# Kernel tuning notes

Hardware: AMD Instinct MI355X
Metric: run time of the kernel (lower is better)

The kernel has to match this reference:

```python
import jax, jax.numpy as jnp
import numpy as np

D_MODEL = 1024
NUM_HEADS = 16
HEAD_DIM = D_MODEL // NUM_HEADS
NUM_KERNELS = 21


def tisa_bias(amp, off, sharp, seq_len):
    # amp/off/sharp: (H, K). Returns (H, L, L) translation-invariant bias.
    # Evaluate on the 2L-1 distinct relative distances, then gather (Toeplitz).
    d = jnp.arange(-(seq_len - 1), seq_len, dtype=amp.dtype)  # (2L-1,)
    # (H, K, 2L-1) -> sum over kernels -> (H, 2L-1)
    scores = jnp.sum(
        amp[:, :, None]
        * jnp.exp(-jnp.abs(sharp)[:, :, None] * (d[None, None, :] - off[:, :, None]) ** 2),
        axis=1,
    )
    i = jnp.arange(seq_len)
    rel_idx = i[None, :] - i[:, None] + (seq_len - 1)  # (L, L) in [0, 2L-2]
    return scores[:, rel_idx]  # (H, L, L)


def setup_inputs() -> dict:
    key = jax.random.key(0)
    ks = jax.random.split(key, 9)
    B, L = 4, 1024
    s = 0.02
    return {
        "x_q": jax.random.normal(ks[0], (B, L, D_MODEL), dtype=jnp.float32),
        "x_kv": jax.random.normal(ks[1], (B, L, D_MODEL), dtype=jnp.float32),
        "Wq": jax.random.normal(ks[2], (D_MODEL, D_MODEL), dtype=jnp.float32) * s,
        "Wm": jax.random.normal(ks[3], (D_MODEL, 2 * D_MODEL), dtype=jnp.float32) * s,
        "Wg": jax.random.normal(ks[4], (D_MODEL, 2 * D_MODEL), dtype=jnp.float32) * s,
        "bg": jnp.zeros((2 * D_MODEL,), dtype=jnp.float32),
        "tisa_amp": jax.random.normal(ks[5], (NUM_HEADS, NUM_KERNELS), dtype=jnp.float32) * 0.1,
        "tisa_off": jax.random.uniform(ks[6], (NUM_HEADS, NUM_KERNELS), dtype=jnp.float32, minval=-512.0, maxval=512.0),
        "tisa_sharp": jax.random.uniform(ks[7], (NUM_HEADS, NUM_KERNELS), dtype=jnp.float32, minval=1e-4, maxval=0.05),
    }


def reference(x_q, x_kv, Wq, Wm, Wg, bg, tisa_amp, tisa_off, tisa_sharp):
    B, Lq, _ = x_q.shape
    Lkv = x_kv.shape[1]
    H, Dh = NUM_HEADS, HEAD_DIM

    q = (x_q @ Wq).reshape(B, Lq, H, Dh).transpose(0, 2, 1, 3)        # (B,H,Lq,Dh)
    mem = (x_kv @ Wm)                                                 # (B,Lkv,2D)
    k = mem[..., :D_MODEL].reshape(B, Lkv, H, Dh).transpose(0, 2, 1, 3)
    v = mem[..., D_MODEL:].reshape(B, Lkv, H, Dh).transpose(0, 2, 1, 3)

    scale = 1.0 / jnp.sqrt(jnp.asarray(Dh, dtype=q.dtype))
    scores = jnp.einsum("bhqd,bhkd->bhqk", q, k) * scale              # (B,H,Lq,Lkv)
    scores = scores + tisa_bias(tisa_amp, tisa_off, tisa_sharp, Lkv)[None]
    weights = jax.nn.softmax(scores, axis=-1)

    attn = jnp.einsum("bhqk,bhkd->bhqd", weights, v)                  # (B,H,Lq,Dh)
    attn = attn.transpose(0, 2, 1, 3).reshape(B, Lq, D_MODEL)

    g = attn @ Wg + bg                                                # (B,Lq,2D)
    a, b = g[..., :D_MODEL], g[..., D_MODEL:]
    return a * jax.nn.sigmoid(b)
```

## Files before the change

kernel.cpp:

```cpp
#include <hip/hip_runtime.h>
#include <cstdint>
#include <cstddef>

typedef __attribute__((ext_vector_type(8))) short bf16x8;
typedef __attribute__((ext_vector_type(4))) float f32x4;

#define LOG2E 1.44269504f

__device__ __forceinline__ unsigned short f2bf(float x) {
  unsigned int u = __float_as_uint(x);
  u += 0x7FFFu + ((u >> 16) & 1u);
  return (unsigned short)(u >> 16);
}
__device__ __forceinline__ unsigned short f2bf_trunc(float x) {
  return (unsigned short)(__float_as_uint(x) >> 16);
}

__device__ __forceinline__ bf16x8 pack8(const float4& a, const float4& b) {
  bf16x8 r;
  r[0] = (short)f2bf(a.x); r[1] = (short)f2bf(a.y);
  r[2] = (short)f2bf(a.z); r[3] = (short)f2bf(a.w);
  r[4] = (short)f2bf(b.x); r[5] = (short)f2bf(b.y);
  r[6] = (short)f2bf(b.z); r[7] = (short)f2bf(b.w);
  return r;
}

__device__ __forceinline__ void gload_lds16(const void* g, void* l) {
  __builtin_amdgcn_global_load_lds(
      (const __attribute__((address_space(1))) unsigned int*)g,
      (__attribute__((address_space(3))) unsigned int*)l, 16, 0, 0);
}


__global__ void preproc(const float* __restrict__ Wq, const float* __restrict__ Wm,
                        const float* __restrict__ Wg,
                        const float* __restrict__ amp, const float* __restrict__ off,
                        const float* __restrict__ sharp,
                        unsigned short* __restrict__ dWq, unsigned short* __restrict__ dWm,
                        unsigned short* __restrict__ dWg, float* __restrict__ tab) {
  __shared__ float tile[32][33];
  const int blk = blockIdx.x;
  if (blk < 6144) {
    int idx = blk;
    int z = idx >> 11, rem = idx & 2047;
    int bx = rem & 63, by = rem >> 6;
    const float* src = z == 0 ? Wq : (z == 1 ? Wm : Wg);
    unsigned short* dst = z == 0 ? dWq : (z == 1 ? dWm : dWg);
    int N = z == 0 ? 1024 : 2048;
    int nb = bx * 32, kb = by * 32;
    if (nb >= N) return;
    int tx = threadIdx.x & 31, ty = threadIdx.x >> 5;
#pragma unroll
    for (int r = ty; r < 32; r += 8)
      tile[r][tx] = src[(size_t)(kb + r) * N + nb + tx];
    __syncthreads();
#pragma unroll
    for (int r = ty; r < 32; r += 8)
      dst[(size_t)(nb + r) * 1024 + kb + tx] = f2bf(tile[tx][r]);
  } else {
    int h = blk - 6144;
    for (int idx = threadIdx.x; idx < 2047; idx += 256) {
      float d = (float)(idx - 1023);
      float acc = 0.f;
#pragma unroll
      for (int k = 0; k < 21; ++k) {
        float dd = d - off[h * 21 + k];
        acc += amp[h * 21 + k] * __expf(-fabsf(sharp[h * 21 + k]) * dd * dd);
      }
      tab[h * 2047 + idx] = acc * LOG2E;
    }
  }
}


template <int MODE>
__global__ __launch_bounds__(256, 3)
void qkv128(const float* __restrict__ X, const unsigned short* __restrict__ WT,
            unsigned short* __restrict__ qbuf, unsigned short* __restrict__ kbuf,
            unsigned short* __restrict__ vtbuf) {
  __shared__ unsigned short sA[3][128 * 32];
  __shared__ unsigned short sB[3][128 * 32];
  const int ntile = blockIdx.y << 7;
  const int mtile = blockIdx.x << 7;
  const int t = threadIdx.x, lane = t & 63, w = t >> 6;
  const int wm = w >> 1, wn = w & 1;
  const int c = lane & 15, g = lane >> 4;

  const int sr = t >> 2;
  const int sch = (t & 3) ^ ((sr >> 1) & 3);
  const float* aP0 = X + (size_t)(mtile + sr) * 1024 + sch * 8;
  const float* aP1 = aP0 + 64 * 1024;
  const unsigned short* bP0 = WT + (size_t)(ntile + sr) * 1024 + sch * 8;
  const unsigned short* bP1 = bP0 + 64 * 1024;
  const int lw = t * 8;

  float4 pA[4], iA[4];
  bf16x8 pB[2], iB[2];
  {
    float4 c0 = *(const float4*)(aP0);
    float4 c1 = *(const float4*)(aP0 + 4);
    float4 c2 = *(const float4*)(aP1);
    float4 c3 = *(const float4*)(aP1 + 4);
    bf16x8 cB0 = *(const bf16x8*)(bP0);
    bf16x8 cB1 = *(const bf16x8*)(bP1);
    pA[0] = *(const float4*)(aP0 + 32);
    pA[1] = *(const float4*)(aP0 + 36);
    pA[2] = *(const float4*)(aP1 + 32);
    pA[3] = *(const float4*)(aP1 + 36);
    pB[0] = *(const bf16x8*)(bP0 + 32);
    pB[1] = *(const bf16x8*)(bP1 + 32);
    *(bf16x8*)&sA[0][lw]        = pack8(c0, c1);
    *(bf16x8*)&sA[0][2048 + lw] = pack8(c2, c3);
    *(bf16x8*)&sB[0][lw]        = cB0;
    *(bf16x8*)&sB[0][2048 + lw] = cB1;
  }
  asm volatile("s_waitcnt lgkmcnt(0)" ::: "memory");
  __builtin_amdgcn_sched_barrier(0);
  asm volatile("s_barrier" ::: "memory");

  const int gx = (g ^ ((c >> 1) & 3)) * 8;
  const int aoff = (wm * 64 + c) * 32 + gx;
  const int boff = (wn * 64 + c) * 32 + gx;

  f32x4 acc[4][4] = {};
  int s0 = 0, s1 = 1, s2 = 2;

  for (int kt = 0; kt < 32; ++kt) {
    if (kt + 2 < 32) {
      const int ko = (kt + 2) * 32;
      iA[0] = *(const float4*)(aP0 + ko);
      iA[1] = *(const float4*)(aP0 + ko + 4);
      iA[2] = *(const float4*)(aP1 + ko);
      iA[3] = *(const float4*)(aP1 + ko + 4);
      iB[0] = *(const bf16x8*)(bP0 + ko);
      iB[1] = *(const bf16x8*)(bP1 + ko);
    }

    const unsigned short* sAp = &sA[s0][0];
    const unsigned short* sBc = &sB[s0][0];
    bf16x8 af[4], bfr[4];
#pragma unroll
    for (int i = 0; i < 4; ++i) af[i]  = *(const bf16x8*)&sAp[aoff + i * 512];
#pragma unroll
    for (int j = 0; j < 4; ++j) bfr[j] = *(const bf16x8*)&sBc[boff + j * 512];

    __builtin_amdgcn_s_setprio(1);
#pragma unroll
    for (int i = 0; i < 4; ++i)
#pragma unroll
      for (int j = 0; j < 4; ++j)
        acc[i][j] = __builtin_amdgcn_mfma_f32_16x16x32_bf16(af[i], bfr[j], acc[i][j], 0, 0, 0);
    __builtin_amdgcn_s_setprio(0);

    if (kt + 1 < 32) {
      *(bf16x8*)&sA[s1][lw]        = pack8(pA[0], pA[1]);
      *(bf16x8*)&sA[s1][2048 + lw] = pack8(pA[2], pA[3]);
      *(bf16x8*)&sB[s1][lw]        = pB[0];
      *(bf16x8*)&sB[s1][2048 + lw] = pB[1];
    }
#pragma unroll
    for (int q = 0; q < 4; ++q) pA[q] = iA[q];
    pB[0] = iB[0]; pB[1] = iB[1];

    asm volatile("s_waitcnt lgkmcnt(0)" ::: "memory");
    __builtin_amdgcn_sched_barrier(0);
    asm volatile("s_barrier" ::: "memory");
    __builtin_amdgcn_sched_barrier(0);

    int tmp = s0; s0 = s1; s1 = s2; s2 = tmp;
  }

  const int row0 = mtile + wm * 64 + (g << 2);
  const int col0 = ntile + wn * 64 + c;
  if (MODE == 0) {
#pragma unroll
    for (int i = 0; i < 4; ++i)
#pragma unroll
      for (int j = 0; j < 4; ++j) {
        int r = row0 + i * 16, cl = col0 + j * 16;
#pragma unroll
        for (int ri = 0; ri < 4; ++ri)
          qbuf[(size_t)(r + ri) * 1024 + cl] = f2bf(acc[i][j][ri] * (0.125f * LOG2E));
      }
  } else if (ntile < 1024) {
#pragma unroll
    for (int i = 0; i < 4; ++i)
#pragma unroll
      for (int j = 0; j < 4; ++j) {
        int r = row0 + i * 16, cl = col0 + j * 16;
#pragma unroll
        for (int ri = 0; ri < 4; ++ri)
          kbuf[(size_t)(r + ri) * 1024 + cl] = f2bf(acc[i][j][ri]);
      }
  } else {
#pragma unroll
    for (int i = 0; i < 4; ++i)
#pragma unroll
      for (int j = 0; j < 4; ++j) {
        int r = row0 + i * 16, cl = col0 + j * 16;
        int d = cl - 1024;
        int hh = d >> 6, dh = d & 63;
        int bb2 = r >> 10, ll = r & 1023;
        ushort4 pk;
        pk.x = f2bf(acc[i][j][0]);
        pk.y = f2bf(acc[i][j][1]);
        pk.z = f2bf(acc[i][j][2]);
        pk.w = f2bf(acc[i][j][3]);
        *(ushort4*)&vtbuf[((size_t)((bb2 * 16 + hh) * 64 + dh) << 10) + ll] = pk;
      }
  }
}


__global__ __launch_bounds__(512)
void attn_kernel(const unsigned short* __restrict__ qbuf,
                 const unsigned short* __restrict__ kbuf,
                 const unsigned short* __restrict__ vtbuf,
                 const float* __restrict__ biasTab,
                 unsigned short* __restrict__ attnb) {
  const int h = blockIdx.x & 15, b = blockIdx.x >> 4, qt = blockIdx.y;
  __shared__ unsigned short sK[2][64 * 64];
  __shared__ unsigned short sV[3][64 * 64];
  __shared__ unsigned short sP[2][128 * 64];
  __shared__ float sLsum[2][128];
  const int t = threadIdx.x, lane = t & 63, w = t >> 6;
  const int c = lane & 15, g = lane >> 4;
  const int rg = w >> 1, cg = w & 1;

  const int r = t >> 3, ch = (t & 7) ^ (r & 7);

  const unsigned short* qsrc = qbuf + (size_t)(b * 1024 + qt * 128) * 1024 + h * 64;
  const unsigned short* ksrc = kbuf + (size_t)(b * 1024) * 1024 + h * 64;
  const unsigned short* vsrc = vtbuf + (size_t)((b * 16 + h) * 64) * 1024;

  unsigned short* sQ = &sP[0][0];
  gload_lds16(qsrc + (size_t)r * 1024 + ch * 8, &sQ[t * 8]);
  gload_lds16(qsrc + (size_t)(r + 64) * 1024 + ch * 8, &sQ[4096 + t * 8]);
  gload_lds16(ksrc + (size_t)r * 1024 + ch * 8, &sK[0][t * 8]);
  gload_lds16(vsrc + (size_t)r * 1024 + ch * 8, &sV[0][t * 8]);

  const float* bb = biasTab + h * 2047 + 1023 + cg * 32 + c - qt * 128 - rg * 32 - g * 4;

  float bc[2][2][4];
#pragma unroll
  for (int rf = 0; rf < 2; ++rf)
#pragma unroll
    for (int nf = 0; nf < 2; ++nf)
#pragma unroll
      for (int ri = 0; ri < 4; ++ri)
        bc[rf][nf][ri] = bb[(nf - rf) * 16 - ri];

  __syncthreads();

  bf16x8 aq[2][2];
#pragma unroll
  for (int rf = 0; rf < 2; ++rf) {
    int row = rg * 32 + rf * 16 + c;
#pragma unroll
    for (int ks = 0; ks < 2; ++ks)
      aq[rf][ks] = *(const bf16x8*)&sQ[row * 64 + (((ks * 4 + g) ^ (row & 7)) * 8)];
  }
  __syncthreads();

  f32x4 o[2][2] = {};
  float lsum[2][4] = {};

  int vcur = 0, vnx = 1;
  for (int kv = 0; kv < 16; ++kv) {
    const int cur = kv & 1;

    f32x4 s[2][2];
#pragma unroll
    for (int rf = 0; rf < 2; ++rf)
#pragma unroll
      for (int nf = 0; nf < 2; ++nf)
#pragma unroll
        for (int ri = 0; ri < 4; ++ri)
          s[rf][nf][ri] = bc[rf][nf][ri];

    if (kv + 1 < 16) {
      gload_lds16(ksrc + (size_t)((kv + 1) * 64 + r) * 1024 + ch * 8, &sK[1 - cur][t * 8]);
      gload_lds16(vsrc + (size_t)r * 1024 + (kv + 1) * 64 + ch * 8, &sV[vnx][t * 8]);
      const float* bk = bb + (kv + 1) * 64;
#pragma unroll
      for (int rf = 0; rf < 2; ++rf)
#pragma unroll
        for (int nf = 0; nf < 2; ++nf)
#pragma unroll
          for (int ri = 0; ri < 4; ++ri)
            bc[rf][nf][ri] = bk[(nf - rf) * 16 - ri];
    }

#pragma unroll
    for (int nf = 0; nf < 2; ++nf) {
      int krow = cg * 32 + nf * 16 + c;
      bf16x8 k0 = *(const bf16x8*)&sK[cur][krow * 64 + (((g) ^ (krow & 7)) * 8)];
      bf16x8 k1 = *(const bf16x8*)&sK[cur][krow * 64 + (((4 + g) ^ (krow & 7)) * 8)];
#pragma unroll
      for (int rf = 0; rf < 2; ++rf) {
        s[rf][nf] = __builtin_amdgcn_mfma_f32_16x16x32_bf16(aq[rf][0], k0, s[rf][nf], 0, 0, 0);
        s[rf][nf] = __builtin_amdgcn_mfma_f32_16x16x32_bf16(aq[rf][1], k1, s[rf][nf], 0, 0, 0);
      }
    }

#pragma unroll
    for (int rf = 0; rf < 2; ++rf)
#pragma unroll
      for (int nf = 0; nf < 2; ++nf)
#pragma unroll
        for (int ri = 0; ri < 4; ++ri) {
          float e = exp2f(s[rf][nf][ri]);
          lsum[rf][ri] += e;
          int prow = rg * 32 + rf * 16 + g * 4 + ri;
          int chunk = cg * 4 + nf * 2 + (c >> 3);
          sP[cur][prow * 64 + ((chunk ^ (prow & 7)) * 8) + (c & 7)] = f2bf_trunc(e);
        }
    __syncthreads();

    bf16x8 ap[2][2];
#pragma unroll
    for (int rf = 0; rf < 2; ++rf) {
      int row = rg * 32 + rf * 16 + c;
#pragma unroll
      for (int ks = 0; ks < 2; ++ks)
        ap[rf][ks] = *(const bf16x8*)&sP[cur][row * 64 + (((ks * 4 + g) ^ (row & 7)) * 8)];
    }
#pragma unroll
    for (int df = 0; df < 2; ++df) {
      int vrow = cg * 32 + df * 16 + c;
      bf16x8 v0 = *(const bf16x8*)&sV[vcur][vrow * 64 + (((g) ^ (vrow & 7)) * 8)];
      bf16x8 v1 = *(const bf16x8*)&sV[vcur][vrow * 64 + (((4 + g) ^ (vrow & 7)) * 8)];
#pragma unroll
      for (int rf = 0; rf < 2; ++rf) {
        o[rf][df] = __builtin_amdgcn_mfma_f32_16x16x32_bf16(ap[rf][0], v0, o[rf][df], 0, 0, 0);
        o[rf][df] = __builtin_amdgcn_mfma_f32_16x16x32_bf16(ap[rf][1], v1, o[rf][df], 0, 0, 0);
      }
    }
    vcur = vnx;
    vnx = (vnx == 2) ? 0 : vnx + 1;
  }

#pragma unroll
  for (int off = 1; off < 16; off <<= 1)
#pragma unroll
    for (int rf = 0; rf < 2; ++rf)
#pragma unroll
      for (int ri = 0; ri < 4; ++ri)
        lsum[rf][ri] += __shfl_xor(lsum[rf][ri], off, 64);
  if (c == 0) {
#pragma unroll
    for (int rf = 0; rf < 2; ++rf)
#pragma unroll
      for (int ri = 0; ri < 4; ++ri)
        sLsum[cg][rg * 32 + rf * 16 + g * 4 + ri] = lsum[rf][ri];
  }
  __syncthreads();

  unsigned short* obase = attnb +
      (size_t)(b * 1024 + qt * 128 + rg * 32 + g * 4) * 1024 + h * 64 + cg * 32 + c;
#pragma unroll
  for (int rf = 0; rf < 2; ++rf)
#pragma unroll
    for (int ri = 0; ri < 4; ++ri) {
      int row = rg * 32 + rf * 16 + g * 4 + ri;
      float rinv = 1.0f / (sLsum[0][row] + sLsum[1][row]);
#pragma unroll
      for (int df = 0; df < 2; ++df)
        obase[(size_t)(rf * 16 + ri) * 1024 + df * 16] = f2bf(o[rf][df][ri] * rinv);
    }
}


__global__ __launch_bounds__(256, 4)
void out_gemm(const unsigned short* __restrict__ A,
              const unsigned short* __restrict__ WgT,
              const float* __restrict__ bg,
              float* __restrict__ out) {
  __shared__ unsigned short sA[2][64 * 32];
  __shared__ unsigned short sB[2][128 * 32];
  const int nb = blockIdx.y;
  const int mtile = blockIdx.x << 6;
  const int t = threadIdx.x, lane = t & 63, w = t >> 6;
  const int c = lane & 15, g = lane >> 4;
  const int rm = w >> 1, cn = w & 1;
  const int srow = t >> 2, scol = (t & 3) << 3;
  const unsigned short* aP = A + (size_t)(mtile + srow) * 1024 + scol;
  const unsigned short* bP0 = WgT + (size_t)(nb * 64 + srow) * 1024 + scol;
  const unsigned short* bP1 = WgT + (size_t)(1024 + nb * 64 + srow) * 1024 + scol;
  const int lo = srow * 32 + scol;

  gload_lds16(aP, &sA[0][lo]);
  gload_lds16(bP0, &sB[0][lo]);
  gload_lds16(bP1, &sB[0][lo + 64 * 32]);
  __syncthreads();

  f32x4 acc[2][4] = {};
  for (int kt = 0; kt < 32; ++kt) {
    const int cur = kt & 1;
    if (kt + 1 < 32) {
      const int ko = (kt + 1) * 32;
      gload_lds16(aP + ko, &sA[1 - cur][lo]);
      gload_lds16(bP0 + ko, &sB[1 - cur][lo]);
      gload_lds16(bP1 + ko, &sB[1 - cur][lo + 64 * 32]);
    }
    bf16x8 af[2], bfr[4];
#pragma unroll
    for (int i = 0; i < 2; ++i)
      af[i] = *(const bf16x8*)&sA[cur][(rm * 32 + i * 16 + c) * 32 + g * 8];
#pragma unroll
    for (int jj = 0; jj < 2; ++jj) {
      bfr[jj]     = *(const bf16x8*)&sB[cur][(cn * 32 + jj * 16 + c) * 32 + g * 8];
      bfr[jj + 2] = *(const bf16x8*)&sB[cur][(64 + cn * 32 + jj * 16 + c) * 32 + g * 8];
    }
#pragma unroll
    for (int i = 0; i < 2; ++i)
#pragma unroll
      for (int j = 0; j < 4; ++j)
        acc[i][j] = __builtin_amdgcn_mfma_f32_16x16x32_bf16(af[i], bfr[j], acc[i][j], 0, 0, 0);
    __syncthreads();
  }

#pragma unroll
  for (int i = 0; i < 2; ++i) {
    int row0 = mtile + rm * 32 + i * 16 + (g << 2);
#pragma unroll
    for (int jj = 0; jj < 2; ++jj) {
      int col = nb * 64 + cn * 32 + jj * 16 + c;
      float ba = bg[col];
      float bbv = bg[1024 + col];
#pragma unroll
      for (int ri = 0; ri < 4; ++ri) {
        float av = acc[i][jj][ri] + ba;
        float bv = acc[i][jj + 2][ri] + bbv;
        out[(size_t)(row0 + ri) * 1024 + col] = av / (1.f + exp2f(-LOG2E * bv));
      }
    }
  }
}


extern "C" void kernel_launch(void* const* d_in, const int* in_sizes, int n_in,
                              void* d_out, int out_size, void* d_ws, size_t ws_size,
                              hipStream_t stream) {
  const float* x_q   = (const float*)d_in[0];
  const float* x_kv  = (const float*)d_in[1];
  const float* Wq    = (const float*)d_in[2];
  const float* Wm    = (const float*)d_in[3];
  const float* Wg    = (const float*)d_in[4];
  const float* bg    = (const float*)d_in[5];
  const float* amp   = (const float*)d_in[6];
  const float* off   = (const float*)d_in[7];
  const float* sharp = (const float*)d_in[8];
  float* out = (float*)d_out;

  char* ws = (char*)d_ws;
  size_t o = 0;
  auto alloc = [&](size_t bytes) {
    char* p = ws + o;
    o += (bytes + 255) & ~(size_t)255;
    return p;
  };
  unsigned short* bWqT  = (unsigned short*)alloc(1024ull * 1024 * 2);
  unsigned short* bWmT  = (unsigned short*)alloc(2048ull * 1024 * 2);
  unsigned short* bWgT  = (unsigned short*)alloc(2048ull * 1024 * 2);
  float*          biasT = (float*)alloc(16ull * 2047 * 4);
  unsigned short* qbuf  = (unsigned short*)alloc(4096ull * 1024 * 2);
  unsigned short* kbuf  = (unsigned short*)alloc(4096ull * 1024 * 2);
  unsigned short* vtbuf = (unsigned short*)alloc(4096ull * 1024 * 2);
  unsigned short* attnb = (unsigned short*)alloc(4096ull * 1024 * 2);
  if (ws_size < o) return;

  preproc<<<6160, 256, 0, stream>>>(Wq, Wm, Wg, amp, off, sharp,
                                    bWqT, bWmT, bWgT, biasT);
  qkv128<0><<<dim3(32, 8), 256, 0, stream>>>(x_q, bWqT, qbuf, nullptr, nullptr);
  qkv128<1><<<dim3(32, 16), 256, 0, stream>>>(x_kv, bWmT, nullptr, kbuf, vtbuf);
  attn_kernel<<<dim3(64, 8), 512, 0, stream>>>(qbuf, kbuf, vtbuf, biasT, attnb);
  out_gemm<<<dim3(64, 16), 256, 0, stream>>>(attnb, bWgT, bg, out);
}
```

Measured before the change: 220.3 us.

## Fuse all stages into one persistent kernel with software grid barriers

Replaces the five separate launches (weight transpose/bias table, Q GEMM, KV GEMM, attention, output GEMM) with a single persistent kernel of 256 blocks that loops over each stage's jobs and synchronises between stages using atomic-counter grid barriers. Tile shapes are adjusted so 512-thread blocks cover the QKV and output GEMMs. This removes launch gaps and per-stage tail effects, but it limits occupancy to one 512-thread block per CU with a large LDS footprint. The barriers rely on all 256 blocks being co-resident, and each one costs global atomics and spinning.

```diff
diff --git a/kernel.cpp b/kernel.cpp
--- a/kernel.cpp
+++ b/kernel.cpp
@@ -31,408 +31,406 @@
       (__attribute__((address_space(3))) unsigned int*)l, 16, 0, 0);
 }
 
-
-__global__ void preproc(const float* __restrict__ Wq, const float* __restrict__ Wm,
-                        const float* __restrict__ Wg,
-                        const float* __restrict__ amp, const float* __restrict__ off,
-                        const float* __restrict__ sharp,
-                        unsigned short* __restrict__ dWq, unsigned short* __restrict__ dWm,
-                        unsigned short* __restrict__ dWg, float* __restrict__ tab) {
-  __shared__ float tile[32][33];
-  const int blk = blockIdx.x;
-  if (blk < 6144) {
-    int idx = blk;
-    int z = idx >> 11, rem = idx & 2047;
-    int bx = rem & 63, by = rem >> 6;
-    const float* src = z == 0 ? Wq : (z == 1 ? Wm : Wg);
-    unsigned short* dst = z == 0 ? dWq : (z == 1 ? dWm : dWg);
-    int N = z == 0 ? 1024 : 2048;
-    int nb = bx * 32, kb = by * 32;
-    if (nb >= N) return;
-    int tx = threadIdx.x & 31, ty = threadIdx.x >> 5;
-#pragma unroll
-    for (int r = ty; r < 32; r += 8)
-      tile[r][tx] = src[(size_t)(kb + r) * N + nb + tx];
-    __syncthreads();
-#pragma unroll
-    for (int r = ty; r < 32; r += 8)
-      dst[(size_t)(nb + r) * 1024 + kb + tx] = f2bf(tile[tx][r]);
-  } else {
-    int h = blk - 6144;
-    for (int idx = threadIdx.x; idx < 2047; idx += 256) {
-      float d = (float)(idx - 1023);
-      float acc = 0.f;
-#pragma unroll
-      for (int k = 0; k < 21; ++k) {
-        float dd = d - off[h * 21 + k];
-        acc += amp[h * 21 + k] * __expf(-fabsf(sharp[h * 21 + k]) * dd * dd);
-      }
-      tab[h * 2047 + idx] = acc * LOG2E;
-    }
+__device__ __forceinline__ void gridbar(unsigned* cells, int phase) {
+  __syncthreads();
+  if (threadIdx.x == 0) {
+    __threadfence();
+    unsigned base = __hip_atomic_load(cells, __ATOMIC_RELAXED, __HIP_MEMORY_SCOPE_AGENT);
+    unsigned* cnt = cells + (phase << 10);
+    __hip_atomic_fetch_add(cnt, 1u, __ATOMIC_ACQ_REL, __HIP_MEMORY_SCOPE_AGENT);
+    unsigned iters = 0;
+    while ((unsigned)(__hip_atomic_load(cnt, __ATOMIC_ACQUIRE, __HIP_MEMORY_SCOPE_AGENT) - base) < 256u) {
+      __builtin_amdgcn_s_sleep(2);
+      if (++iters > 20000000u) break;
+    }
+    __threadfence();
   }
-}
-
-
-template <int MODE>
-__global__ __launch_bounds__(256, 3)
-void qkv128(const float* __restrict__ X, const unsigned short* __restrict__ WT,
-            unsigned short* __restrict__ qbuf, unsigned short* __restrict__ kbuf,
-            unsigned short* __restrict__ vtbuf) {
-  __shared__ unsigned short sA[3][128 * 32];
-  __shared__ unsigned short sB[3][128 * 32];
-  const int ntile = blockIdx.y << 7;
-  const int mtile = blockIdx.x << 7;
-  const int t = threadIdx.x, lane = t & 63, w = t >> 6;
-  const int wm = w >> 1, wn = w & 1;
-  const int c = lane & 15, g = lane >> 4;
-
-  const int sr = t >> 2;
-  const int sch = (t & 3) ^ ((sr >> 1) & 3);
-  const float* aP0 = X + (size_t)(mtile + sr) * 1024 + sch * 8;
-  const float* aP1 = aP0 + 64 * 1024;
-  const unsigned short* bP0 = WT + (size_t)(ntile + sr) * 1024 + sch * 8;
-  const unsigned short* bP1 = bP0 + 64 * 1024;
-  const int lw = t * 8;
-
-  float4 pA[4], iA[4];
-  bf16x8 pB[2], iB[2];
-  {
-    float4 c0 = *(const float4*)(aP0);
-    float4 c1 = *(const float4*)(aP0 + 4);
-    float4 c2 = *(const float4*)(aP1);
-    float4 c3 = *(const float4*)(aP1 + 4);
-    bf16x8 cB0 = *(const bf16x8*)(bP0);
-    bf16x8 cB1 = *(const bf16x8*)(bP1);
-    pA[0] = *(const float4*)(aP0 + 32);
-    pA[1] = *(const float4*)(aP0 + 36);
-    pA[2] = *(const float4*)(aP1 + 32);
-    pA[3] = *(const float4*)(aP1 + 36);
-    pB[0] = *(const bf16x8*)(bP0 + 32);
-    pB[1] = *(const bf16x8*)(bP1 + 32);
-    *(bf16x8*)&sA[0][lw]        = pack8(c0, c1);
-    *(bf16x8*)&sA[0][2048 + lw] = pack8(c2, c3);
-    *(bf16x8*)&sB[0][lw]        = cB0;
-    *(bf16x8*)&sB[0][2048 + lw] = cB1;
-  }
-  asm volatile("s_waitcnt lgkmcnt(0)" ::: "memory");
-  __builtin_amdgcn_sched_barrier(0);
-  asm volatile("s_barrier" ::: "memory");
-
-  const int gx = (g ^ ((c >> 1) & 3)) * 8;
-  const int aoff = (wm * 64 + c) * 32 + gx;
-  const int boff = (wn * 64 + c) * 32 + gx;
-
-  f32x4 acc[4][4] = {};
-  int s0 = 0, s1 = 1, s2 = 2;
-
-  for (int kt = 0; kt < 32; ++kt) {
-    if (kt + 2 < 32) {
-      const int ko = (kt + 2) * 32;
-      iA[0] = *(const float4*)(aP0 + ko);
-      iA[1] = *(const float4*)(aP0 + ko + 4);
-      iA[2] = *(const float4*)(aP1 + ko);
-      iA[3] = *(const float4*)(aP1 + ko + 4);
-      iB[0] = *(const bf16x8*)(bP0 + ko);
-      iB[1] = *(const bf16x8*)(bP1 + ko);
-    }
-
-    const unsigned short* sAp = &sA[s0][0];
-    const unsigned short* sBc = &sB[s0][0];
-    bf16x8 af[4], bfr[4];
-#pragma unroll
-    for (int i = 0; i < 4; ++i) af[i]  = *(const bf16x8*)&sAp[aoff + i * 512];
-#pragma unroll
-    for (int j = 0; j < 4; ++j) bfr[j] = *(const bf16x8*)&sBc[boff + j * 512];
-
-    __builtin_amdgcn_s_setprio(1);
-#pragma unroll
-    for (int i = 0; i < 4; ++i)
-#pragma unroll
-      for (int j = 0; j < 4; ++j)
-        acc[i][j] = __builtin_amdgcn_mfma_f32_16x16x32_bf16(af[i], bfr[j], acc[i][j], 0, 0, 0);
-    __builtin_amdgcn_s_setprio(0);
-
-    if (kt + 1 < 32) {
-      *(bf16x8*)&sA[s1][lw]        = pack8(pA[0], pA[1]);
-      *(bf16x8*)&sA[s1][2048 + lw] = pack8(pA[2], pA[3]);
-      *(bf16x8*)&sB[s1][lw]        = pB[0];
-      *(bf16x8*)&sB[s1][2048 + lw] = pB[1];
-    }
-#pragma unroll
-    for (int q = 0; q < 4; ++q) pA[q] = iA[q];
-    pB[0] = iB[0]; pB[1] = iB[1];
-
-    asm volatile("s_waitcnt lgkmcnt(0)" ::: "memory");
-    __builtin_amdgcn_sched_barrier(0);
-    asm volatile("s_barrier" ::: "memory");
-    __builtin_amdgcn_sched_barrier(0);
-
-    int tmp = s0; s0 = s1; s1 = s2; s2 = tmp;
-  }
-
-  const int row0 = mtile + wm * 64 + (g << 2);
-  const int col0 = ntile + wn * 64 + c;
-  if (MODE == 0) {
-#pragma unroll
-    for (int i = 0; i < 4; ++i)
-#pragma unroll
-      for (int j = 0; j < 4; ++j) {
-        int r = row0 + i * 16, cl = col0 + j * 16;
-#pragma unroll
-        for (int ri = 0; ri < 4; ++ri)
-          qbuf[(size_t)(r + ri) * 1024 + cl] = f2bf(acc[i][j][ri] * (0.125f * LOG2E));
-      }
-  } else if (ntile < 1024) {
-#pragma unroll
-    for (int i = 0; i < 4; ++i)
-#pragma unroll
-      for (int j = 0; j < 4; ++j) {
-        int r = row0 + i * 16, cl = col0 + j * 16;
-#pragma unroll
-        for (int ri = 0; ri < 4; ++ri)
-          kbuf[(size_t)(r + ri) * 1024 + cl] = f2bf(acc[i][j][ri]);
-      }
-  } else {
-#pragma unroll
-    for (int i = 0; i < 4; ++i)
-#pragma unroll
-      for (int j = 0; j < 4; ++j) {
-        int r = row0 + i * 16, cl = col0 + j * 16;
-        int d = cl - 1024;
-        int hh = d >> 6, dh = d & 63;
-        int bb2 = r >> 10, ll = r & 1023;
-        ushort4 pk;
-        pk.x = f2bf(acc[i][j][0]);
-        pk.y = f2bf(acc[i][j][1]);
-        pk.z = f2bf(acc[i][j][2]);
-        pk.w = f2bf(acc[i][j][3]);
-        *(ushort4*)&vtbuf[((size_t)((bb2 * 16 + hh) * 64 + dh) << 10) + ll] = pk;
-      }
-  }
+  __syncthreads();
 }
 
 
 __global__ __launch_bounds__(512)
-void attn_kernel(const unsigned short* __restrict__ qbuf,
-                 const unsigned short* __restrict__ kbuf,
-                 const unsigned short* __restrict__ vtbuf,
-                 const float* __restrict__ biasTab,
-                 unsigned short* __restrict__ attnb) {
-  const int h = blockIdx.x & 15, b = blockIdx.x >> 4, qt = blockIdx.y;
-  __shared__ unsigned short sK[2][64 * 64];
-  __shared__ unsigned short sV[3][64 * 64];
-  __shared__ unsigned short sP[2][128 * 64];
-  __shared__ float sLsum[2][128];
+void mega(const float* __restrict__ x_q, const float* __restrict__ x_kv,
+          const float* __restrict__ Wq, const float* __restrict__ Wm,
+          const float* __restrict__ Wg, const float* __restrict__ bg,
+          const float* __restrict__ amp, const float* __restrict__ off,
+          const float* __restrict__ sharp,
+          unsigned short* __restrict__ bWqT, unsigned short* __restrict__ bWmT,
+          unsigned short* __restrict__ bWgT, float* __restrict__ biasT,
+          unsigned short* __restrict__ qbuf, unsigned short* __restrict__ kbuf,
+          unsigned short* __restrict__ vtbuf, unsigned short* __restrict__ attnb,
+          float* __restrict__ out, unsigned* cells) {
+  __shared__ __align__(16) char smem[90112];
+  const int bid = blockIdx.x;
   const int t = threadIdx.x, lane = t & 63, w = t >> 6;
   const int c = lane & 15, g = lane >> 4;
-  const int rg = w >> 1, cg = w & 1;
-
-  const int r = t >> 3, ch = (t & 7) ^ (r & 7);
-
-  const unsigned short* qsrc = qbuf + (size_t)(b * 1024 + qt * 128) * 1024 + h * 64;
-  const unsigned short* ksrc = kbuf + (size_t)(b * 1024) * 1024 + h * 64;
-  const unsigned short* vsrc = vtbuf + (size_t)((b * 16 + h) * 64) * 1024;
-
-  unsigned short* sQ = &sP[0][0];
-  gload_lds16(qsrc + (size_t)r * 1024 + ch * 8, &sQ[t * 8]);
-  gload_lds16(qsrc + (size_t)(r + 64) * 1024 + ch * 8, &sQ[4096 + t * 8]);
-  gload_lds16(ksrc + (size_t)r * 1024 + ch * 8, &sK[0][t * 8]);
-  gload_lds16(vsrc + (size_t)r * 1024 + ch * 8, &sV[0][t * 8]);
-
-  const float* bb = biasTab + h * 2047 + 1023 + cg * 32 + c - qt * 128 - rg * 32 - g * 4;
-
-  float bc[2][2][4];
-#pragma unroll
-  for (int rf = 0; rf < 2; ++rf)
-#pragma unroll
-    for (int nf = 0; nf < 2; ++nf)
-#pragma unroll
-      for (int ri = 0; ri < 4; ++ri)
-        bc[rf][nf][ri] = bb[(nf - rf) * 16 - ri];
-
-  __syncthreads();
-
-  bf16x8 aq[2][2];
-#pragma unroll
-  for (int rf = 0; rf < 2; ++rf) {
-    int row = rg * 32 + rf * 16 + c;
-#pragma unroll
-    for (int ks = 0; ks < 2; ++ks)
-      aq[rf][ks] = *(const bf16x8*)&sQ[row * 64 + (((ks * 4 + g) ^ (row & 7)) * 8)];
+
+  {
+    float* tile = (float*)smem;
+    const int tx = t & 31, ty = t >> 5;
+#pragma unroll 1
+    for (int k = 0; k < 24; ++k) {
+      const int jid = bid * 24 + k;
+      const int z = jid >> 11, rem = jid & 2047;
+      const int bx = rem & 63, by = rem >> 6;
+      const float* src = z == 0 ? Wq : (z == 1 ? Wm : Wg);
+      unsigned short* dst = z == 0 ? bWqT : (z == 1 ? bWmT : bWgT);
+      const int N = z == 0 ? 1024 : 2048;
+      const int nb = bx * 32, kb = by * 32;
+      if (nb < N) {
+        tile[ty * 33 + tx]        = src[(size_t)(kb + ty) * N + nb + tx];
+        tile[(ty + 16) * 33 + tx] = src[(size_t)(kb + ty + 16) * N + nb + tx];
+        __syncthreads();
+        dst[(size_t)(nb + ty) * 1024 + kb + tx]        = f2bf(tile[tx * 33 + ty]);
+        dst[(size_t)(nb + ty + 16) * 1024 + kb + tx]   = f2bf(tile[tx * 33 + ty + 16]);
+        __syncthreads();
+      }
+    }
+    if (bid < 16) {
+      const int h = bid;
+      for (int idx = t; idx < 2047; idx += 512) {
+        float d = (float)(idx - 1023);
+        float acc = 0.f;
+#pragma unroll
+        for (int kk = 0; kk < 21; ++kk) {
+          float dd = d - off[h * 21 + kk];
+          acc += amp[h * 21 + kk] * __expf(-fabsf(sharp[h * 21 + kk]) * dd * dd);
+        }
+        biasT[h * 2047 + idx] = acc * LOG2E;
+      }
+    }
   }
-  __syncthreads();
-
-  f32x4 o[2][2] = {};
-  float lsum[2][4] = {};
-
-  int vcur = 0, vnx = 1;
-  for (int kv = 0; kv < 16; ++kv) {
-    const int cur = kv & 1;
-
-    f32x4 s[2][2];
-#pragma unroll
-    for (int rf = 0; rf < 2; ++rf)
-#pragma unroll
-      for (int nf = 0; nf < 2; ++nf)
-#pragma unroll
-        for (int ri = 0; ri < 4; ++ri)
-          s[rf][nf][ri] = bc[rf][nf][ri];
-
-    if (kv + 1 < 16) {
-      gload_lds16(ksrc + (size_t)((kv + 1) * 64 + r) * 1024 + ch * 8, &sK[1 - cur][t * 8]);
-      gload_lds16(vsrc + (size_t)r * 1024 + (kv + 1) * 64 + ch * 8, &sV[vnx][t * 8]);
-      const float* bk = bb + (kv + 1) * 64;
+  gridbar(cells, 1);
+
+  {
+    unsigned short* sA = (unsigned short*)smem;
+    unsigned short* sB = (unsigned short*)(smem + 24576);
+    const int wm = w >> 2, wn = w & 3;
+    const int sr = t >> 2;
+    const int sch = (t & 3) ^ ((sr >> 1) & 3);
+    const int lw = t * 8;
+    const int gx = (g ^ ((c >> 1) & 3)) * 8;
+    const int aoff = (wm * 64 + c) * 32 + gx;
+    const int boff = (wn * 32 + c) * 32 + gx;
+#pragma unroll 1
+    for (int kjob = 0; kjob < 3; ++kjob) {
+      const int jid = bid + kjob * 256;
+      const bool isQ = jid < 256;
+      const int jr = isQ ? jid : jid - 256;
+      const int m = isQ ? (jr >> 3) : (jr >> 4);
+      const int n = isQ ? (jr & 7) : (jr & 15);
+      const float* X = isQ ? x_q : x_kv;
+      const unsigned short* WT = isQ ? bWqT : bWmT;
+      const int mtile = m << 7, ntile = n << 7;
+      const float* aP = X + (size_t)(mtile + sr) * 1024 + sch * 8;
+      const unsigned short* bP = WT + (size_t)(ntile + sr) * 1024 + sch * 8;
+
+      float4 pA0, pA1, iA0, iA1;
+      bf16x8 pB, iB;
+      {
+        float4 c0 = *(const float4*)(aP);
+        float4 c1 = *(const float4*)(aP + 4);
+        bf16x8 cB = *(const bf16x8*)(bP);
+        pA0 = *(const float4*)(aP + 32);
+        pA1 = *(const float4*)(aP + 36);
+        pB  = *(const bf16x8*)(bP + 32);
+        *(bf16x8*)&sA[lw] = pack8(c0, c1);
+        *(bf16x8*)&sB[lw] = cB;
+      }
+      asm volatile("s_waitcnt lgkmcnt(0)" ::: "memory");
+      __builtin_amdgcn_sched_barrier(0);
+      asm volatile("s_barrier" ::: "memory");
+
+      f32x4 acc[4][2] = {};
+      int s0 = 0, s1 = 4096, s2 = 8192;
+#pragma unroll 1
+      for (int kt = 0; kt < 32; ++kt) {
+        if (kt + 2 < 32) {
+          const int ko = (kt + 2) * 32;
+          iA0 = *(const float4*)(aP + ko);
+          iA1 = *(const float4*)(aP + ko + 4);
+          iB  = *(const bf16x8*)(bP + ko);
+        }
+        bf16x8 af[4], bfr[2];
+#pragma unroll
+        for (int i = 0; i < 4; ++i) af[i]  = *(const bf16x8*)&sA[s0 + aoff + i * 512];
+#pragma unroll
+        for (int j = 0; j < 2; ++j) bfr[j] = *(const bf16x8*)&sB[s0 + boff + j * 512];
+        __builtin_amdgcn_s_setprio(1);
+#pragma unroll
+        for (int i = 0; i < 4; ++i)
+#pragma unroll
+          for (int j = 0; j < 2; ++j)
+            acc[i][j] = __builtin_amdgcn_mfma_f32_16x16x32_bf16(af[i], bfr[j], acc[i][j], 0, 0, 0);
+        __builtin_amdgcn_s_setprio(0);
+        if (kt + 1 < 32) {
+          *(bf16x8*)&sA[s1 + lw] = pack8(pA0, pA1);
+          *(bf16x8*)&sB[s1 + lw] = pB;
+        }
+        pA0 = iA0; pA1 = iA1; pB = iB;
+        asm volatile("s_waitcnt lgkmcnt(0)" ::: "memory");
+        __builtin_amdgcn_sched_barrier(0);
+        asm volatile("s_barrier" ::: "memory");
+        __builtin_amdgcn_sched_barrier(0);
+        int tmp = s0; s0 = s1; s1 = s2; s2 = tmp;
+      }
+
+      const int row0 = mtile + wm * 64 + (g << 2);
+      const int col0 = ntile + wn * 32 + c;
+      if (isQ) {
+#pragma unroll
+        for (int i = 0; i < 4; ++i)
+#pragma unroll
+          for (int j = 0; j < 2; ++j) {
+            int r2 = row0 + i * 16, cl = col0 + j * 16;
+#pragma unroll
+            for (int ri = 0; ri < 4; ++ri)
+              qbuf[(size_t)(r2 + ri) * 1024 + cl] = f2bf(acc[i][j][ri] * (0.125f * LOG2E));
+          }
+      } else if (ntile < 1024) {
+#pragma unroll
+        for (int i = 0; i < 4; ++i)
+#pragma unroll
+          for (int j = 0; j < 2; ++j) {
+            int r2 = row0 + i * 16, cl = col0 + j * 16;
+#pragma unroll
+            for (int ri = 0; ri < 4; ++ri)
+              kbuf[(size_t)(r2 + ri) * 1024 + cl] = f2bf(acc[i][j][ri]);
+          }
+      } else {
+#pragma unroll
+        for (int i = 0; i < 4; ++i)
+#pragma unroll
+          for (int j = 0; j < 2; ++j) {
+            int r2 = row0 + i * 16, cl = col0 + j * 16;
+            int d = cl - 1024;
+            int hh = d >> 6, dh = d & 63;
+            int bb2 = r2 >> 10, ll = r2 & 1023;
+            ushort4 pk;
+            pk.x = f2bf(acc[i][j][0]);
+            pk.y = f2bf(acc[i][j][1]);
+            pk.z = f2bf(acc[i][j][2]);
+            pk.w = f2bf(acc[i][j][3]);
+            *(ushort4*)&vtbuf[((size_t)((bb2 * 16 + hh) * 64 + dh) << 10) + ll] = pk;
+          }
+      }
+    }
+  }
+  gridbar(cells, 2);
+
+  {
+    unsigned short* sK = (unsigned short*)smem;
+    unsigned short* sV = (unsigned short*)(smem + 16384);
+    unsigned short* sP = (unsigned short*)(smem + 40960);
+    float* sLsum = (float*)(smem + 73728);
+    const int rg = w >> 1, cg = w & 1;
+    const int r = t >> 3, ch = (t & 7) ^ (r & 7);
+#pragma unroll 1
+    for (int kjob = 0; kjob < 2; ++kjob) {
+      const int jid = bid + kjob * 256;
+      const int h = jid & 15, b = (jid >> 4) & 3, qt = jid >> 6;
+
+      const unsigned short* qsrc = qbuf + (size_t)(b * 1024 + qt * 128) * 1024 + h * 64;
+      const unsigned short* ksrc = kbuf + (size_t)(b * 1024) * 1024 + h * 64;
+      const unsigned short* vsrc = vtbuf + (size_t)((b * 16 + h) * 64) * 1024;
+
+      unsigned short* sQ = sP;
+      gload_lds16(qsrc + (size_t)r * 1024 + ch * 8, &sQ[t * 8]);
+      gload_lds16(qsrc + (size_t)(r + 64) * 1024 + ch * 8, &sQ[4096 + t * 8]);
+      gload_lds16(ksrc + (size_t)r * 1024 + ch * 8, &sK[t * 8]);
+      gload_lds16(vsrc + (size_t)r * 1024 + ch * 8, &sV[t * 8]);
+
+      const float* bb = biasT + h * 2047 + 1023 + cg * 32 + c - qt * 128 - rg * 32 - g * 4;
+      float bc[2][2][4];
 #pragma unroll
       for (int rf = 0; rf < 2; ++rf)
 #pragma unroll
         for (int nf = 0; nf < 2; ++nf)
 #pragma unroll
           for (int ri = 0; ri < 4; ++ri)
-            bc[rf][nf][ri] = bk[(nf - rf) * 16 - ri];
-    }
-
-#pragma unroll
-    for (int nf = 0; nf < 2; ++nf) {
-      int krow = cg * 32 + nf * 16 + c;
-      bf16x8 k0 = *(const bf16x8*)&sK[cur][krow * 64 + (((g) ^ (krow & 7)) * 8)];
-      bf16x8 k1 = *(const bf16x8*)&sK[cur][krow * 64 + (((4 + g) ^ (krow & 7)) * 8)];
+            bc[rf][nf][ri] = bb[(nf - rf) * 16 - ri];
+
+      __syncthreads();
+
+      bf16x8 aq[2][2];
 #pragma unroll
       for (int rf = 0; rf < 2; ++rf) {
-        s[rf][nf] = __builtin_amdgcn_mfma_f32_16x16x32_bf16(aq[rf][0], k0, s[rf][nf], 0, 0, 0);
-        s[rf][nf] = __builtin_amdgcn_mfma_f32_16x16x32_bf16(aq[rf][1], k1, s[rf][nf], 0, 0, 0);
-      }
-    }
-
-#pragma unroll
-    for (int rf = 0; rf < 2; ++rf)
-#pragma unroll
-      for (int nf = 0; nf < 2; ++nf)
+        int row = rg * 32 + rf * 16 + c;
+#pragma unroll
+        for (int ks = 0; ks < 2; ++ks)
+          aq[rf][ks] = *(const bf16x8*)&sQ[row * 64 + (((ks * 4 + g) ^ (row & 7)) * 8)];
+      }
+      __syncthreads();
+
+      f32x4 o[2][2] = {};
+      float lsum[2][4] = {};
+      int vcur = 0, vnx = 1;
+#pragma unroll 1
+      for (int kv = 0; kv < 16; ++kv) {
+        const int cur = kv & 1;
+        f32x4 s[2][2];
+#pragma unroll
+        for (int rf = 0; rf < 2; ++rf)
+#pragma unroll
+          for (int nf = 0; nf < 2; ++nf)
+#pragma unroll
+            for (int ri = 0; ri < 4; ++ri)
+              s[rf][nf][ri] = bc[rf][nf][ri];
+
+        if (kv + 1 < 16) {
+          gload_lds16(ksrc + (size_t)((kv + 1) * 64 + r) * 1024 + ch * 8, &sK[(1 - cur) * 4096 + t * 8]);
+          gload_lds16(vsrc + (size_t)r * 1024 + (kv + 1) * 64 + ch * 8, &sV[vnx * 4096 + t * 8]);
+          const float* bk = bb + (kv + 1) * 64;
+#pragma unroll
+          for (int rf = 0; rf < 2; ++rf)
+#pragma unroll
+            for (int nf = 0; nf < 2; ++nf)
+#pragma unroll
+              for (int ri = 0; ri < 4; ++ri)
+                bc[rf][nf][ri] = bk[(nf - rf) * 16 - ri];
+        }
+
+#pragma unroll
+        for (int nf = 0; nf < 2; ++nf) {
+          int krow = cg * 32 + nf * 16 + c;
+          bf16x8 k0 = *(const bf16x8*)&sK[cur * 4096 + krow * 64 + (((g) ^ (krow & 7)) * 8)];
+          bf16x8 k1 = *(const bf16x8*)&sK[cur * 4096 + krow * 64 + (((4 + g) ^ (krow & 7)) * 8)];
+#pragma unroll
+          for (int rf = 0; rf < 2; ++rf) {
+            s[rf][nf] = __builtin_amdgcn_mfma_f32_16x16x32_bf16(aq[rf][0], k0, s[rf][nf], 0, 0, 0);
+            s[rf][nf] = __builtin_amdgcn_mfma_f32_16x16x32_bf16(aq[rf][1], k1, s[rf][nf], 0, 0, 0);
+          }
+        }
+
+#pragma unroll
+        for (int rf = 0; rf < 2; ++rf)
+#pragma unroll
+          for (int nf = 0; nf < 2; ++nf)
+#pragma unroll
+            for (int ri = 0; ri < 4; ++ri) {
+              float e = exp2f(s[rf][nf][ri]);
+              lsum[rf][ri] += e;
+              int prow = rg * 32 + rf * 16 + g * 4 + ri;
+              int chunk = cg * 4 + nf * 2 + (c >> 3);
+              sP[cur * 8192 + prow * 64 + ((chunk ^ (prow & 7)) * 8) + (c & 7)] = f2bf_trunc(e);
+            }
+        __syncthreads();
+
+        bf16x8 ap[2][2];
+#pragma unroll
+        for (int rf = 0; rf < 2; ++rf) {
+          int row = rg * 32 + rf * 16 + c;
+#pragma unroll
+          for (int ks = 0; ks < 2; ++ks)
+            ap[rf][ks] = *(const bf16x8*)&sP[cur * 8192 + row * 64 + (((ks * 4 + g) ^ (row & 7)) * 8)];
+        }
+#pragma unroll
+        for (int df = 0; df < 2; ++df) {
+          int vrow = cg * 32 + df * 16 + c;
+          bf16x8 v0 = *(const bf16x8*)&sV[vcur * 4096 + vrow * 64 + (((g) ^ (vrow & 7)) * 8)];
+          bf16x8 v1 = *(const bf16x8*)&sV[vcur * 4096 + vrow * 64 + (((4 + g) ^ (vrow & 7)) * 8)];
+#pragma unroll
+          for (int rf = 0; rf < 2; ++rf) {
+            o[rf][df] = __builtin_amdgcn_mfma_f32_16x16x32_bf16(ap[rf][0], v0, o[rf][df], 0, 0, 0);
+            o[rf][df] = __builtin_amdgcn_mfma_f32_16x16x32_bf16(ap[rf][1], v1, o[rf][df], 0, 0, 0);
+          }
+        }
+        vcur = vnx;
+        vnx = (vnx == 2) ? 0 : vnx + 1;
+      }
+
+#pragma unroll
+      for (int offx = 1; offx < 16; offx <<= 1)
+#pragma unroll
+        for (int rf = 0; rf < 2; ++rf)
+#pragma unroll
+          for (int ri = 0; ri < 4; ++ri)
+            lsum[rf][ri] += __shfl_xor(lsum[rf][ri], offx, 64);
+      if (c == 0) {
+#pragma unroll
+        for (int rf = 0; rf < 2; ++rf)
+#pragma unroll
+          for (int ri = 0; ri < 4; ++ri)
+            sLsum[cg * 128 + rg * 32 + rf * 16 + g * 4 + ri] = lsum[rf][ri];
+      }
+      __syncthreads();
+
+      unsigned short* obase = attnb +
+          (size_t)(b * 1024 + qt * 128 + rg * 32 + g * 4) * 1024 + h * 64 + cg * 32 + c;
+#pragma unroll
+      for (int rf = 0; rf < 2; ++rf)
 #pragma unroll
         for (int ri = 0; ri < 4; ++ri) {
-          float e = exp2f(s[rf][nf][ri]);
-          lsum[rf][ri] += e;
-          int prow = rg * 32 + rf * 16 + g * 4 + ri;
-          int chunk = cg * 4 + nf * 2 + (c >> 3);
-          sP[cur][prow * 64 + ((chunk ^ (prow & 7)) * 8) + (c & 7)] = f2bf_trunc(e);
-        }
-    __syncthreads();
-
-    bf16x8 ap[2][2];
-#pragma unroll
-    for (int rf = 0; rf < 2; ++rf) {
-      int row = rg * 32 + rf * 16 + c;
-#pragma unroll
-      for (int ks = 0; ks < 2; ++ks)
-        ap[rf][ks] = *(const bf16x8*)&sP[cur][row * 64 + (((ks * 4 + g) ^ (row & 7)) * 8)];
-    }
-#pragma unroll
-    for (int df = 0; df < 2; ++df) {
-      int vrow = cg * 32 + df * 16 + c;
-      bf16x8 v0 = *(const bf16x8*)&sV[vcur][vrow * 64 + (((g) ^ (vrow & 7)) * 8)];
-      bf16x8 v1 = *(const bf16x8*)&sV[vcur][vrow * 64 + (((4 + g) ^ (vrow & 7)) * 8)];
-#pragma unroll
-      for (int rf = 0; rf < 2; ++rf) {
-        o[rf][df] = __builtin_amdgcn_mfma_f32_16x16x32_bf16(ap[rf][0], v0, o[rf][df], 0, 0, 0);
-        o[rf][df] = __builtin_amdgcn_mfma_f32_16x16x32_bf16(ap[rf][1], v1, o[rf][df], 0, 0, 0);
-      }
-    }
-    vcur = vnx;
-    vnx = (vnx == 2) ? 0 : vnx + 1;
+          int row = rg * 32 + rf * 16 + g * 4 + ri;
+          float rinv = 1.0f / (sLsum[0 * 128 + row] + sLsum[1 * 128 + row]);
+#pragma unroll
+          for (int df = 0; df < 2; ++df)
+            obase[(size_t)(rf * 16 + ri) * 1024 + df * 16] = f2bf(o[rf][df][ri] * rinv);
+        }
+    }
   }
-
-#pragma unroll
-  for (int off = 1; off < 16; off <<= 1)
-#pragma unroll
-    for (int rf = 0; rf < 2; ++rf)
-#pragma unroll
-      for (int ri = 0; ri < 4; ++ri)
-        lsum[rf][ri] += __shfl_xor(lsum[rf][ri], off, 64);
-  if (c == 0) {
-#pragma unroll
-    for (int rf = 0; rf < 2; ++rf)
-#pragma unroll
-      for (int ri = 0; ri < 4; ++ri)
-        sLsum[cg][rg * 32 + rf * 16 + g * 4 + ri] = lsum[rf][ri];
-  }
-  __syncthreads();
-
-  unsigned short* obase = attnb +
-      (size_t)(b * 1024 + qt * 128 + rg * 32 + g * 4) * 1024 + h * 64 + cg * 32 + c;
-#pragma unroll
-  for (int rf = 0; rf < 2; ++rf)
-#pragma unroll
-    for (int ri = 0; ri < 4; ++ri) {
-      int row = rg * 32 + rf * 16 + g * 4 + ri;
-      float rinv = 1.0f / (sLsum[0][row] + sLsum[1][row]);
-#pragma unroll
-      for (int df = 0; df < 2; ++df)
-        obase[(size_t)(rf * 16 + ri) * 1024 + df * 16] = f2bf(o[rf][df][ri] * rinv);
-    }
-}
-
-
-__global__ __launch_bounds__(256, 4)
-void out_gemm(const unsigned short* __restrict__ A,
-              const unsigned short* __restrict__ WgT,
-              const float* __restrict__ bg,
-              float* __restrict__ out) {
-  __shared__ unsigned short sA[2][64 * 32];
-  __shared__ unsigned short sB[2][128 * 32];
-  const int nb = blockIdx.y;
-  const int mtile = blockIdx.x << 6;
-  const int t = threadIdx.x, lane = t & 63, w = t >> 6;
-  const int c = lane & 15, g = lane >> 4;
-  const int rm = w >> 1, cn = w & 1;
-  const int srow = t >> 2, scol = (t & 3) << 3;
-  const unsigned short* aP = A + (size_t)(mtile + srow) * 1024 + scol;
-  const unsigned short* bP0 = WgT + (size_t)(nb * 64 + srow) * 1024 + scol;
-  const unsigned short* bP1 = WgT + (size_t)(1024 + nb * 64 + srow) * 1024 + scol;
-  const int lo = srow * 32 + scol;
-
-  gload_lds16(aP, &sA[0][lo]);
-  gload_lds16(bP0, &sB[0][lo]);
-  gload_lds16(bP1, &sB[0][lo + 64 * 32]);
-  __syncthreads();
-
-  f32x4 acc[2][4] = {};
-  for (int kt = 0; kt < 32; ++kt) {
-    const int cur = kt & 1;
-    if (kt + 1 < 32) {
-      const int ko = (kt + 1) * 32;
-      gload_lds16(aP + ko, &sA[1 - cur][lo]);
-      gload_lds16(bP0 + ko, &sB[1 - cur][lo]);
-      gload_lds16(bP1 + ko, &sB[1 - cur][lo + 64 * 32]);
-    }
-    bf16x8 af[2], bfr[4];
-#pragma unroll
-    for (int i = 0; i < 2; ++i)
-      af[i] = *(const bf16x8*)&sA[cur][(rm * 32 + i * 16 + c) * 32 + g * 8];
-#pragma unroll
-    for (int jj = 0; jj < 2; ++jj) {
-      bfr[jj]     = *(const bf16x8*)&sB[cur][(cn * 32 + jj * 16 + c) * 32 + g * 8];
-      bfr[jj + 2] = *(const bf16x8*)&sB[cur][(64 + cn * 32 + jj * 16 + c) * 32 + g * 8];
-    }
-#pragma unroll
-    for (int i = 0; i < 2; ++i)
-#pragma unroll
-      for (int j = 0; j < 4; ++j)
-        acc[i][j] = __builtin_amdgcn_mfma_f32_16x16x32_bf16(af[i], bfr[j], acc[i][j], 0, 0, 0);
-    __syncthreads();
-  }
-
-#pragma unroll
-  for (int i = 0; i < 2; ++i) {
-    int row0 = mtile + rm * 32 + i * 16 + (g << 2);
-#pragma unroll
-    for (int jj = 0; jj < 2; ++jj) {
-      int col = nb * 64 + cn * 32 + jj * 16 + c;
-      float ba = bg[col];
-      float bbv = bg[1024 + col];
-#pragma unroll
-      for (int ri = 0; ri < 4; ++ri) {
-        float av = acc[i][jj][ri] + ba;
-        float bv = acc[i][jj + 2][ri] + bbv;
-        out[(size_t)(row0 + ri) * 1024 + col] = av / (1.f + exp2f(-LOG2E * bv));
+  gridbar(cells, 3);
+
+  {
+    unsigned short* sA = (unsigned short*)smem;
+    unsigned short* sB = (unsigned short*)(smem + 16384);
+    const int rm = w >> 1, cn = w & 1;
+    const int srow = t >> 2, scol = (t & 3) << 3;
+    const int lo = srow * 32 + scol;
+#pragma unroll 1
+    for (int kjob = 0; kjob < 2; ++kjob) {
+      const int jid = bid + kjob * 256;
+      const int m = jid >> 4, nb = jid & 15;
+      const int mtile = m << 7;
+      const unsigned short* aP = attnb + (size_t)(mtile + srow) * 1024 + scol;
+      const int bRow = (srow < 64) ? (nb * 64 + srow) : (1024 + nb * 64 + srow - 64);
+      const unsigned short* bP = bWgT + (size_t)bRow * 1024 + scol;
+
+      gload_lds16(aP, &sA[lo]);
+      gload_lds16(bP, &sB[lo]);
+      __syncthreads();
+
+      f32x4 acc[2][4] = {};
+#pragma unroll 1
+      for (int kt = 0; kt < 32; ++kt) {
+        const int cur = kt & 1;
+        if (kt + 1 < 32) {
+          const int ko = (kt + 1) * 32;
+          gload_lds16(aP + ko, &sA[(1 - cur) * 4096 + lo]);
+          gload_lds16(bP + ko, &sB[(1 - cur) * 4096 + lo]);
+        }
+        bf16x8 af[2], bfr[4];
+#pragma unroll
+        for (int i = 0; i < 2; ++i)
+          af[i] = *(const bf16x8*)&sA[cur * 4096 + (rm * 32 + i * 16 + c) * 32 + g * 8];
+#pragma unroll
+        for (int jj = 0; jj < 2; ++jj) {
+          bfr[jj]     = *(const bf16x8*)&sB[cur * 4096 + (cn * 32 + jj * 16 + c) * 32 + g * 8];
+          bfr[jj + 2] = *(const bf16x8*)&sB[cur * 4096 + (64 + cn * 32 + jj * 16 + c) * 32 + g * 8];
+        }
+#pragma unroll
+        for (int i = 0; i < 2; ++i)
+#pragma unroll
+          for (int j = 0; j < 4; ++j)
+            acc[i][j] = __builtin_amdgcn_mfma_f32_16x16x32_bf16(af[i], bfr[j], acc[i][j], 0, 0, 0);
+        __syncthreads();
+      }
+
+#pragma unroll
+      for (int i = 0; i < 2; ++i) {
+        int row0 = mtile + rm * 32 + i * 16 + (g << 2);
+#pragma unroll
+        for (int jj = 0; jj < 2; ++jj) {
+          int col = nb * 64 + cn * 32 + jj * 16 + c;
+          float ba = bg[col];
+          float bbv = bg[1024 + col];
+#pragma unroll
+          for (int ri = 0; ri < 4; ++ri) {
+            float av = acc[i][jj][ri] + ba;
+            float bv = acc[i][jj + 2][ri] + bbv;
+            out[(size_t)(row0 + ri) * 1024 + col] = av / (1.f + exp2f(-LOG2E * bv));
+          }
+        }
       }
     }
   }
@@ -468,12 +466,10 @@
   unsigned short* kbuf  = (unsigned short*)alloc(4096ull * 1024 * 2);
   unsigned short* vtbuf = (unsigned short*)alloc(4096ull * 1024 * 2);
   unsigned short* attnb = (unsigned short*)alloc(4096ull * 1024 * 2);
+  unsigned*       cells = (unsigned*)alloc(16384);
   if (ws_size < o) return;
 
-  preproc<<<6160, 256, 0, stream>>>(Wq, Wm, Wg, amp, off, sharp,
-                                    bWqT, bWmT, bWgT, biasT);
-  qkv128<0><<<dim3(32, 8), 256, 0, stream>>>(x_q, bWqT, qbuf, nullptr, nullptr);
-  qkv128<1><<<dim3(32, 16), 256, 0, stream>>>(x_kv, bWmT, nullptr, kbuf, vtbuf);
-  attn_kernel<<<dim3(64, 8), 512, 0, stream>>>(qbuf, kbuf, vtbuf, biasT, attnb);
-  out_gemm<<<dim3(64, 16), 256, 0, stream>>>(attnb, bWgT, bg, out);
-}
+  mega<<<256, 512, 0, stream>>>(x_q, x_kv, Wq, Wm, Wg, bg, amp, off, sharp,
+                                bWqT, bWmT, bWgT, biasT,
+                                qbuf, kbuf, vtbuf, attnb, out, cells);
+}
```

Result: slower. 409.3 us (+85.8%).
